# Performance work log

Measured on AMD Instinct MI355X. Metric: run time of the kernel, lower is better.

The kernel has to match this reference:

```python
import jax, jax.numpy as jnp
import numpy as np

B, M, N, R, FIN, D, H = 16, 512, 512, 8, 4, 256, 4
DH = D // H
LGAT = 2
TF_RATE, THRESH = 0.9, 2.0
GAT_W, ORG_W, DET_W = 0.5, 0.5, 0.5


def setup_inputs() -> dict:
    key = jax.random.key(0)
    ks = jax.random.split(key, 16)
    g = lambda k, shp, fan: jax.random.normal(k, shp, jnp.float32) / np.sqrt(fan)
    inp = {
        'tracks': jax.random.normal(ks[0], (B, M, R, FIN), jnp.float32),
        'detections': jax.random.normal(ks[1], (B, N, FIN), jnp.float32),
        'tracklet_marks': jax.random.randint(ks[2], (B,), M // 2, M + 1, jnp.int32),
        'detection_marks': jax.random.randint(ks[3], (B,), N // 2, N + 1, jnp.int32),
        'feat_W1': g(ks[4], (FIN, D), FIN),
        'feat_b1': jnp.zeros((D,), jnp.float32),
        'feat_W2': g(ks[5], (D, D), D),
        'feat_b2': jnp.zeros((D,), jnp.float32),
        'enc_Wqkv': g(ks[6], (D, 3 * D), D),
        'enc_Wo': g(ks[7], (D, D), D),
        'enc_ff1': g(ks[8], (D, 4 * D), D),
        'enc_ff2': g(ks[9], (4 * D, D), 4 * D),
        'gat_W': g(ks[10], (LGAT, D, D), D),
        'gat_a': g(ks[11], (LGAT, 2, H, DH), DH),
        'det_gat_W': g(ks[12], (LGAT, D, D), D),
        'det_gat_a': g(ks[13], (LGAT, 2, H, DH), DH),
        'cls_Wq': g(ks[14], (2, D, D), D),
        'cls_Wk': g(ks[15], (2, D, D), D),
    }
    return inp


def _ln(x):
    m = jnp.mean(x, -1, keepdims=True)
    v = jnp.var(x, -1, keepdims=True)
    return (x - m) * jax.lax.rsqrt(v + 1e-5)


def _feat(x, W1, b1, W2, b2):
    return jax.nn.elu(x @ W1 + b1) @ W2 + b2


def _encoder(x, Wqkv, Wo, ff1, ff2):
    # x: [T, R, D] -> one pre-LN transformer layer over the rewind axis
    T = x.shape[0]
    h = _ln(x)
    qkv = (h @ Wqkv).reshape(T, R, 3, H, DH)
    q, k, v = qkv[:, :, 0], qkv[:, :, 1], qkv[:, :, 2]
    att = jax.nn.softmax(jnp.einsum('trhd,tshd->thrs', q, k) / np.sqrt(DH), axis=-1)
    o = jnp.einsum('thrs,tshd->trhd', att, v).reshape(T, R, D) @ Wo
    x = x + o
    return x + jax.nn.relu(_ln(x) @ ff1) @ ff2


def _gat(x, adj, W, a):
    # x: [B, Nn, D]; adj: [B, Nn, Nn] bool; a: [2, H, DH]
    b, nn_, _ = x.shape
    h = (x @ W).reshape(b, nn_, H, DH)
    src = jnp.einsum('bnhd,hd->bnh', h, a[0])
    dst = jnp.einsum('bnhd,hd->bnh', h, a[1])
    e = jax.nn.leaky_relu(src[:, :, None, :] + dst[:, None, :, :], 0.2)  # [B,Nn,Nn,H]
    e = jnp.where(adj[..., None], e, -1e9)
    alpha = jax.nn.softmax(e, axis=2)
    out = jnp.einsum('bijh,bjhd->bihd', alpha, h).reshape(b, nn_, D)
    return jax.nn.elu(out)


def _scores(x, adj_f, Wq, Wk):
    s = jax.nn.sigmoid(jnp.einsum('bid,bjd->bij', x @ Wq, x @ Wk) / np.sqrt(D))
    return s * adj_f


def _forward(tracks, detections, tracklet_marks, detection_marks,
             feat_W1, feat_b1, feat_W2, feat_b2,
             enc_Wqkv, enc_Wo, enc_ff1, enc_ff2,
             gat_W, gat_a, det_gat_W, det_gat_a, cls_Wq, cls_Wk):
    tr_emb = _feat(tracks, feat_W1, feat_b1, feat_W2, feat_b2)      # [B,M,R,D]
    det_emb = _feat(detections, feat_W1, feat_b1, feat_W2, feat_b2)  # [B,N,D]

    enc = _encoder(tr_emb.reshape(B * M, R, D), enc_Wqkv, enc_Wo, enc_ff1, enc_ff2)
    enc = enc.reshape(B, M, R, D)
    predicted = tr_emb[:, :, 0, :] + TF_RATE * enc[:, :, 0, :]       # [B,M,D]

    tmask = jnp.arange(M)[None, :] < tracklet_marks[:, None]
    dmask = jnp.arange(N)[None, :] < detection_marks[:, None]

    pos = jnp.concatenate([tracks[:, :, 0, :2], detections[:, :, :2]], axis=1)  # [B,M+N,2]
    vmask = jnp.concatenate([tmask, dmask], axis=1)
    dist = jnp.linalg.norm(pos[:, :, None, :] - pos[:, None, :, :], axis=-1)
    adj = (dist < THRESH) & vmask[:, :, None] & vmask[:, None, :]
    adj_f = adj.astype(jnp.float32)

    feat0 = jnp.concatenate([predicted, det_emb], axis=1)  # [B,M+N,D]
    x = feat0
    for l in range(LGAT):
        x = GAT_W * _gat(x, adj, gat_W[l], gat_a[l]) + ORG_W * feat0
    scores = _scores(x, adj_f, cls_Wq[0], cls_Wk[0])       # [B,M+N,M+N]
    asso_results = scores[:, :M, M:]                        # track->det block

    pd = detections[:, :, :2]
    dist_d = jnp.linalg.norm(pd[:, :, None, :] - pd[:, None, :, :], axis=-1)
    adj_d = (dist_d < THRESH) & dmask[:, :, None] & dmask[:, None, :]
    adj_d_f = adj_d.astype(jnp.float32)

    xd = det_emb
    for l in range(LGAT):
        xd = DET_W * _gat(xd, adj_d, det_gat_W[l], det_gat_a[l]) + ORG_W * det_emb
    det_scores = _scores(xd, adj_d_f, cls_Wq[1], cls_Wk[1])
    det_scores = det_scores * (1.0 - jnp.eye(N, dtype=jnp.float32))  # zero_diag

    return scores, det_scores, asso_results


def reference(tracks, detections, tracklet_marks, detection_marks,
              feat_W1, feat_b1, feat_W2, feat_b2,
              enc_Wqkv, enc_Wo, enc_ff1, enc_ff2,
              gat_W, gat_a, det_gat_W, det_gat_a, cls_Wq, cls_Wk):
    return _forward(tracks, detections, tracklet_marks, detection_marks,
                    feat_W1, feat_b1, feat_W2, feat_b2,
                    enc_Wqkv, enc_Wo, enc_ff1, enc_ff2,
                    gat_W, gat_a, det_gat_W, det_gat_a, cls_Wq, cls_Wk)
```

## Files before the change

kernel.cpp:

```cpp
#include <hip/hip_runtime.h>
#include <math.h>


typedef __bf16 bf16;
typedef __bf16 bf16x8 __attribute__((ext_vector_type(8)));
typedef __bf16 bf16x4 __attribute__((ext_vector_type(4)));
typedef float f32x4 __attribute__((ext_vector_type(4)));

__device__ __forceinline__ float bf2f(bf16 x) { return (float)x; }
__device__ __forceinline__ bf16 f2bf(float x) { return (bf16)x; }

__device__ __forceinline__ unsigned encf(float f) {
    unsigned u = __float_as_uint(f);
    return (u & 0x80000000u) ? ~u : (u | 0x80000000u);
}
__device__ __forceinline__ float decf(unsigned u) {
    return (u & 0x80000000u) ? __uint_as_float(u & 0x7fffffffu)
                             : __uint_as_float(~u);
}

__device__ __forceinline__ bool node_adj(float4 a, float4 c) {
    float dx = a.x - c.x, dy = a.y - c.y;
    return (sqrtf(dx * dx + dy * dy) + a.z + c.z) < 2.0f;
}
// ... 8 lines not shown
    int k = 0;
    #pragma unroll
    for (int q = 1; q < 13; ++q) if (tid >= tab.e[q].tstart) k = q;
    PrepEnt E = tab.e[k];
    const int local = tid - E.tstart;
    const int cT = E.C >> 5;
    const int tr = local / cT, tc = local - tr * cT;
    const int r0 = tr << 5, c0 = tc << 5;
    const int t = threadIdx.x;
    {
        int r = t >> 3, cq = (t & 7) * 4;
        *(float4*)&tile[r][cq] = *(const float4*)(E.src + (long)(r0 + r) * E.C + c0 + cq);
    }
    __syncthreads();
    {
        int c = t >> 3, rq = (t & 7) * 4;
        bf16x4 o;
        o[0] = f2bf(tile[rq + 0][c]); o[1] = f2bf(tile[rq + 1][c]);
        o[2] = f2bf(tile[rq + 2][c]); o[3] = f2bf(tile[rq + 3][c]);
        *(bf16x4*)(dst + E.dofs + (long)(c0 + c) * E.R + r0 + rq) = o;
    }
}

__device__ __forceinline__ void gemm_bt(const bf16* __restrict__ A, int lda,
                                        const bf16* __restrict__ BT, int ldb,
                                        int K, f32x4 acc[4])
{
    __shared__ bf16 As[64][40];
    __shared__ bf16 Bs[64][40];
    const int t = threadIdx.x;
    const int m0 = blockIdx.y * 64;
    const int n0 = blockIdx.x * 64;
    const int lane = t & 63, wv = t >> 6, lr = lane & 15, kq = lane >> 4;
    const int arow = t >> 2, acol = (t & 3) * 8;
    for (int k0 = 0; k0 < K; k0 += 32) {
        __syncthreads();
        *(uint4*)&As[arow][acol] = *(const uint4*)(A + (long)(m0 + arow) * lda + k0 + acol);
        *(uint4*)&Bs[arow][acol] = *(const uint4*)(BT + (long)(n0 + arow) * ldb + k0 + acol);
        __syncthreads();
        bf16x8 af = *(const bf16x8*)&As[wv * 16 + lr][kq * 8];
        #pragma unroll
        for (int nt = 0; nt < 4; ++nt) {
            bf16x8 bfr = *(const bf16x8*)&Bs[nt * 16 + lr][kq * 8];
            acc[nt] = __builtin_amdgcn_mfma_f32_16x16x32_bf16(af, bfr, acc[nt], 0, 0, 0);
        }
    }
}

__device__ __forceinline__ void gemm128_core(const bf16* __restrict__ A, int lda,
                                             const bf16* __restrict__ BT, int ldb,
                                             int m0, int n0, int K, f32x4 acc[2][8])
{
    __shared__ bf16 As[128][40];
    __shared__ bf16 Bs[128][40];
    const int t = threadIdx.x;
    const int lane = t & 63, wv = t >> 6, lr = lane & 15, kq = lane >> 4;
    const int srow = t >> 1, scol = (t & 1) * 16;
    for (int k0 = 0; k0 < K; k0 += 32) {
        __syncthreads();
        {
            const bf16* ap = A + (long)(m0 + srow) * lda + k0 + scol;
            *(uint4*)&As[srow][scol] = *(const uint4*)ap;
            *(uint4*)&As[srow][scol + 8] = *(const uint4*)(ap + 8);
            const bf16* bp = BT + (long)(n0 + srow) * ldb + k0 + scol;
            *(uint4*)&Bs[srow][scol] = *(const uint4*)bp;
            *(uint4*)&Bs[srow][scol + 8] = *(const uint4*)(bp + 8);
        }
        __syncthreads();
        bf16x8 af[2];
// ... 14 lines not shown
    bf16* __restrict__ out, int ldo, int K, int relu)
{
    f32x4 acc[2][8] = {};
    const int m0 = blockIdx.y * 128, n0 = blockIdx.x * 128;
    gemm128_core(A, lda, BT, ldb, m0, n0, K, acc);
    const int lane = threadIdx.x & 63, wv = threadIdx.x >> 6;
    const int lr = lane & 15, kq = lane >> 4;
    #pragma unroll
    for (int mt = 0; mt < 2; ++mt) {
        #pragma unroll
        for (int nt = 0; nt < 8; ++nt) {
            int col = n0 + nt * 16 + lr;
            #pragma unroll
            for (int i = 0; i < 4; ++i) {
                int row = m0 + wv * 32 + mt * 16 + kq * 4 + i;
                float v = acc[mt][nt][i];
                if (relu) v = fmaxf(v, 0.f);
                out[(long)row * ldo + col] = f2bf(v);
            }
        }
    }
}

__global__ __launch_bounds__(256) void k_gemm128_logits(
    const bf16* __restrict__ xqk, long sAz, int K,
    float* __restrict__ out, int ldo, long sOz,
    const unsigned long long* __restrict__ adjm, int nN, int nC,
    float* __restrict__ asso, int flags)
{
    f32x4 acc[2][8] = {};
    const int z = blockIdx.z;
    const int m0 = blockIdx.y * 128, n0 = blockIdx.x * 128;
    gemm128_core(xqk + z * sAz, 512, xqk + z * sAz + 256, 512, m0, n0, K, acc);
    const int lane = threadIdx.x & 63, wv = threadIdx.x >> 6;
    const int lr = lane & 15, kq = lane >> 4;
    float* ob = out + z * sOz;
    #pragma unroll
    for (int mt = 0; mt < 2; ++mt) {
        #pragma unroll
        for (int i = 0; i < 4; ++i) {
            int row = m0 + wv * 32 + mt * 16 + kq * 4 + i;
            unsigned long long w0 = adjm[((long)z * nN + row) * nC + (n0 >> 6)];
            unsigned long long w1 = adjm[((long)z * nN + row) * nC + (n0 >> 6) + 1];
            #pragma unroll
            for (int nt = 0; nt < 8; ++nt) {
                int col = n0 + nt * 16 + lr;
                int bp = nt * 16 + lr;
                bool adj = (bp < 64) ? ((w0 >> bp) & 1ull) : ((w1 >> (bp - 64)) & 1ull);
                if ((flags & 2) && row == col) adj = false;
                float v = 0.f;
                if (adj) v = 1.f / (1.f + __expf(-acc[mt][nt][i] * 0.0625f));
                ob[(long)row * ldo + col] = v;
                if ((flags & 1) && row < 512 && col >= 512)
                    asso[(long)z * 262144 + (long)row * 512 + (col - 512)] = v;
            }
        }
    }
}

__global__ __launch_bounds__(256) void k_gemm_bf16(
    const bf16* __restrict__ A, int lda,
    const bf16* __restrict__ BT, int ldb,
    bf16* __restrict__ out, int ldo, int K, int relu)
{
    f32x4 acc[4] = {};
    gemm_bt(A, lda, BT, ldb, K, acc);
    const int lane = threadIdx.x & 63, wv = threadIdx.x >> 6;
    const int lr = lane & 15, kq = lane >> 4;
    const int m0 = blockIdx.y * 64, n0 = blockIdx.x * 64;
    #pragma unroll
    for (int nt = 0; nt < 4; ++nt) {
        int col = n0 + nt * 16 + lr;
        #pragma unroll
        for (int i = 0; i < 4; ++i) {
            int row = m0 + wv * 16 + kq * 4 + i;
            float v = acc[nt][i];
            if (relu) v = fmaxf(v, 0.f);
            out[(long)row * ldo + col] = f2bf(v);
        }
    }
}

__global__ __launch_bounds__(256) void k_gemm_addres(
    const bf16* __restrict__ A, int lda,
    const bf16* __restrict__ BT, int ldb,
    const float* __restrict__ res1, int ldr1,
    float* __restrict__ outf, int ldo, int K)
{
    f32x4 acc[4] = {};
    gemm_bt(A, lda, BT, ldb, K, acc);
    const int lane = threadIdx.x & 63, wv = threadIdx.x >> 6;
    const int lr = lane & 15, kq = lane >> 4;
    const int m0 = blockIdx.y * 64, n0 = blockIdx.x * 64;
    #pragma unroll
    for (int nt = 0; nt < 4; ++nt) {
        int col = n0 + nt * 16 + lr;
        #pragma unroll
        for (int i = 0; i < 4; ++i) {
            int row = m0 + wv * 16 + kq * 4 + i;
            outf[(long)row * ldo + col] = res1[(long)row * ldr1 + col] + acc[nt][i];
        }
    }
}

__global__ __launch_bounds__(256) void k_gemm_pred(
    const bf16* __restrict__ A, int lda,
    const bf16* __restrict__ BT, int ldb,
    const float* __restrict__ res1, const float* __restrict__ res2,
    float* __restrict__ outf, bf16* __restrict__ outb, int K)
{
    f32x4 acc[4] = {};
    gemm_bt(A, lda, BT, ldb, K, acc);
    const int lane = threadIdx.x & 63, wv = threadIdx.x >> 6;
    const int lr = lane & 15, kq = lane >> 4;
    const int m0 = blockIdx.y * 64, n0 = blockIdx.x * 64;
    #pragma unroll
    for (int nt = 0; nt < 4; ++nt) {
        int col = n0 + nt * 16 + lr;
        #pragma unroll
        for (int i = 0; i < 4; ++i) {
            int row = m0 + wv * 16 + kq * 4 + i;
            float v = res1[(long)row * 256 + col]
                    + 0.9f * (res2[(long)row * 256 + col] + acc[nt][i]);
            long drow = (long)row + ((row >> 9) << 9);
            long o = drow * 256 + col;
            outf[o] = v;
            outb[o] = f2bf(v);
        }
    }
}

__global__ __launch_bounds__(256) void k_gemm_T(
    const bf16* __restrict__ WT, const bf16* __restrict__ X,
    bf16* __restrict__ hgT, int nN, int nLog)
{
    f32x4 acc[4] = {};
    gemm_bt(WT, 256, X, 256, 256, acc);
    const int lane = threadIdx.x & 63, wv = threadIdx.x >> 6;
    const int lr = lane & 15, kq = lane >> 4;
    const int d0 = blockIdx.y * 64, n0 = blockIdx.x * 64;
    #pragma unroll
    for (int nt = 0; nt < 4; ++nt) {
        int node = n0 + nt * 16 + lr;
        int b = node >> nLog;
        int j = node & (nN - 1);
        #pragma unroll
        for (int i = 0; i < 4; ++i) {
            int d = d0 + wv * 16 + kq * 4 + i;
            hgT[((long)(b * 256 + d) << nLog) + j] = f2bf(acc[nt][i]);
        }
    }
}

__global__ __launch_bounds__(256) void k_featgemm(
    const float* __restrict__ tracks, const float* __restrict__ dets,
    const float* __restrict__ W1, const float* __restrict__ b1,
    const bf16* __restrict__ W2T, const float* __restrict__ b2,
    bf16* __restrict__ emb_b, float* __restrict__ emb_r0_f,
    float* __restrict__ feat0_f, bf16* __restrict__ feat0_b,
    bf16* __restrict__ demb_b)
{
    __shared__ float xr[64][4];
    __shared__ float w1s[4][256];
    __shared__ float b1s[256];
    __shared__ bf16 As[64][40];
    __shared__ bf16 Bs[256][40];
    const int t = threadIdx.x;
    const int m0 = blockIdx.x * 64;
    if (t < 64) {
        int gr = m0 + t;
        const float* sp = (gr < 65536) ? (tracks + (long)gr * 4)
                                       : (dets + (long)(gr - 65536) * 4);
        *(float4*)&xr[t][0] = *(const float4*)sp;
    }
    w1s[0][t] = W1[t];       w1s[1][t] = W1[256 + t];
    w1s[2][t] = W1[512 + t]; w1s[3][t] = W1[768 + t];
    b1s[t] = b1[t];
    const int arow = t >> 2, acol = (t & 3) * 8;
    const int lane = t & 63, wv = t >> 6, lr = lane & 15, kq = lane >> 4;
    f32x4 acc[16] = {};
    __syncthreads();
// ... 2 lines not shown
        #pragma unroll
        for (int j = 0; j < 8; ++j) {
            int c = k0 + acol + j;
            float v = fmaf(xr[arow][0], w1s[0][c],
                      fmaf(xr[arow][1], w1s[1][c],
                      fmaf(xr[arow][2], w1s[2][c],
                      fmaf(xr[arow][3], w1s[3][c], b1s[c]))));
            v = v > 0.f ? v : (__expf(v) - 1.f);
            As[arow][acol + j] = f2bf(v);
        }
        #pragma unroll
        for (int rr = 0; rr < 4; ++rr) {
            int n = rr * 64 + (t >> 2);
            *(uint4*)&Bs[n][acol] = *(const uint4*)(W2T + (long)n * 256 + k0 + acol);
        }
        __syncthreads();
        bf16x8 af = *(const bf16x8*)&As[wv * 16 + lr][kq * 8];
        #pragma unroll
        for (int nt = 0; nt < 16; ++nt) {
            bf16x8 bfr = *(const bf16x8*)&Bs[nt * 16 + lr][kq * 8];
            acc[nt] = __builtin_amdgcn_mfma_f32_16x16x32_bf16(af, bfr, acc[nt], 0, 0, 0);
        }
    }
    #pragma unroll
    for (int nt = 0; nt < 16; ++nt) {
        int col = nt * 16 + lr;
        float bv = b2[col];
        #pragma unroll
        for (int i = 0; i < 4; ++i) {
            int gr = m0 + wv * 16 + kq * 4 + i;
            float v = acc[nt][i] + bv;
            emb_b[(long)gr * 256 + col] = f2bf(v);
            if (gr < 65536) {
                if ((gr & 7) == 0) emb_r0_f[(long)(gr >> 3) * 256 + col] = v;
            } else {
                int dr = gr - 65536;
                long drow = ((long)(dr >> 9) << 10) + 512 + (dr & 511);
                feat0_f[drow * 256 + col] = v;
                feat0_b[drow * 256 + col] = f2bf(v);
                demb_b[(long)dr * 256 + col] = f2bf(v);
            }
        }
    }
}

__global__ __launch_bounds__(256) void k_adjmask(
    const float4* __restrict__ nodes,
    unsigned long long* __restrict__ adjm_main,
    unsigned long long* __restrict__ adjm_det)
{
    int bi, nN, nLog, nodeOfs;
    unsigned long long* adjm;
    if (blockIdx.x < 16384) { bi = blockIdx.x; nN = 1024; nLog = 10; nodeOfs = 0; adjm = adjm_main; }
    else { bi = blockIdx.x - 16384; nN = 512; nLog = 9; nodeOfs = 512; adjm = adjm_det; }
    const int b = bi >> nLog;
    const int i = bi & (nN - 1);
    const float4* nb = nodes + b * 1024 + nodeOfs;
    const float4 ni = nb[i];
    const int t = threadIdx.x;
    const int w = t >> 6, lane = t & 63;
    const int nC = nN >> 6;
    for (int it = 0; it * 256 < nN; ++it) {
        int j = it * 256 + t;
        bool adj = node_adj(ni, nb[j]);
        unsigned long long mask = __ballot(adj);
        if (lane == 0) adjm[(long)bi * nC + it * 4 + w] = mask;
    }
}

__global__ __launch_bounds__(256) void k_ln_bf16(const bf16* __restrict__ x, bf16* __restrict__ out)
{
    const int w = threadIdx.x >> 6, l = threadIdx.x & 63;
    const long row = (long)blockIdx.x * 4 + w;
    bf16x4 xv = *(const bf16x4*)(x + row * 256 + l * 4);
    float v0 = bf2f(xv[0]), v1 = bf2f(xv[1]), v2 = bf2f(xv[2]), v3 = bf2f(xv[3]);
    float s = v0 + v1 + v2 + v3;
    #pragma unroll
    for (int o = 32; o; o >>= 1) s += __shfl_xor(s, o, 64);
    float mean = s * (1.f / 256.f);
    float d0 = v0 - mean, d1 = v1 - mean, d2 = v2 - mean, d3 = v3 - mean;
    float q = d0 * d0 + d1 * d1 + d2 * d2 + d3 * d3;
    #pragma unroll
    for (int o = 32; o; o >>= 1) q += __shfl_xor(q, o, 64);
    float rstd = rsqrtf(q * (1.f / 256.f) + 1e-5f);
    bf16x4 ov;
    ov[0] = f2bf(d0 * rstd); ov[1] = f2bf(d1 * rstd);
    ov[2] = f2bf(d2 * rstd); ov[3] = f2bf(d3 * rstd);
    *(bf16x4*)(out + row * 256 + l * 4) = ov;
}

__global__ __launch_bounds__(256) void k_ln_f32(const float* __restrict__ x, bf16* __restrict__ out)
{
    const int w = threadIdx.x >> 6, l = threadIdx.x & 63;
    const long row = (long)blockIdx.x * 4 + w;
    float4 xv = *(const float4*)(x + row * 256 + l * 4);
    float s = xv.x + xv.y + xv.z + xv.w;
    #pragma unroll
    for (int o = 32; o; o >>= 1) s += __shfl_xor(s, o, 64);
    float mean = s * (1.f / 256.f);
    float d0 = xv.x - mean, d1 = xv.y - mean, d2 = xv.z - mean, d3 = xv.w - mean;
    float q = d0 * d0 + d1 * d1 + d2 * d2 + d3 * d3;
    #pragma unroll
    for (int o = 32; o; o >>= 1) q += __shfl_xor(q, o, 64);
    float rstd = rsqrtf(q * (1.f / 256.f) + 1e-5f);
    bf16x4 ov;
    ov[0] = f2bf(d0 * rstd); ov[1] = f2bf(d1 * rstd);
    ov[2] = f2bf(d2 * rstd); ov[3] = f2bf(d3 * rstd);
    *(bf16x4*)(out + row * 256 + l * 4) = ov;
}

__global__ __launch_bounds__(256) void k_attn(
    const bf16* __restrict__ q, const bf16* __restrict__ kv,
    bf16* __restrict__ o0)
{
    const long t = blockIdx.x;
    const int h = threadIdx.x >> 6;
    const int lane = threadIdx.x & 63;
    const int s = lane >> 3;
    const int dg = lane & 7;
    const bf16* qp = q + t * 256 + h * 64 + dg * 8;
    const bf16* kp = kv + (t * 8 + s) * 512 + h * 64 + dg * 8;
    float p = 0.f;
    #pragma unroll
    for (int e = 0; e < 8; ++e) p += bf2f(qp[e]) * bf2f(kp[e]);
    p += __shfl_xor(p, 1, 64);
    p += __shfl_xor(p, 2, 64);
    p += __shfl_xor(p, 4, 64);
    float sc = p * 0.125f;
    float w[8];
    float mx = -1e30f;
    #pragma unroll
// ... 13 lines not shown
    const float* __restrict__ tracks, const float* __restrict__ dets,
    const int* __restrict__ tm, const int* __restrict__ dm,
    float4* __restrict__ nodes, unsigned* __restrict__ maxd_all)
{
    int idx = blockIdx.x * 256 + threadIdx.x;
    if (blockIdx.x == 0) maxd_all[threadIdx.x] = 0x007fffffu;
    int b = idx >> 10;
    int i = idx & 1023;
    float x, y;
    int valid;
    if (i < 512) {
        long o = (long)(b * 512 + i) * 32;
        x = tracks[o]; y = tracks[o + 1];
        valid = (i < tm[b]) ? 1 : 0;
    } else {
        int n = i - 512;
        long o = (long)(b * 512 + n) * 4;
        x = dets[o]; y = dets[o + 1];
        valid = (n < dm[b]) ? 1 : 0;
    }
    nodes[idx] = make_float4(x, y, valid ? 0.f : 1e9f, 0.f);
}

__global__ __launch_bounds__(256) void k_srcdst_T(
    const bf16* __restrict__ hgT, const float* __restrict__ av,
    float* __restrict__ src, float* __restrict__ dst,
    unsigned* __restrict__ maxd_enc, int nN, int nLog)
{
    __shared__ float avs[512];
    const int t = threadIdx.x;
    avs[t] = av[t]; avs[256 + t] = av[256 + t];
    __syncthreads();
    const int jl = t & 63, h = t >> 6;
    const int n = blockIdx.x * 64 + jl;
    const int b = n >> nLog, j = n & (nN - 1);
    const bf16* base = hgT + (((long)b * 256 + h * 64) << nLog) + j;
    float p0 = 0.f, p1 = 0.f;
    #pragma unroll 8
    for (int dd = 0; dd < 64; ++dd) {
        float v = bf2f(base[(long)dd << nLog]);
        p0 += v * avs[h * 64 + dd];
        p1 += v * avs[256 + h * 64 + dd];
    }
    src[(long)n * 4 + h] = p0;
    dst[(long)n * 4 + h] = p1;
    float m = p1;
    #pragma unroll
    for (int o = 32; o; o >>= 1) m = fmaxf(m, __shfl_xor(m, o, 64));
    if (jl == 0) atomicMax(&maxd_enc[b * 4 + h], encf(m));
}

__global__ __launch_bounds__(256) void k_gatagg_mm(
    const bf16* __restrict__ hgT,
    const unsigned long long* __restrict__ adjm,
    const float4* __restrict__ srcv, const unsigned* __restrict__ maxd_enc,
    const float4* __restrict__ dstv,
    const float* __restrict__ res, int resBatchStride,
    bf16* __restrict__ outb, int nN)
{
    __shared__ float dstT[4][1024];
    __shared__ unsigned int adjW[32][33];
    const int t = threadIdx.x;
    const int nblk = nN >> 5;
    const int b = blockIdx.x / nblk;
    const int i0 = (blockIdx.x - b * nblk) << 5;
    const int nC = nN >> 6;
    for (int j = t; j < nN; j += 256) {
        float4 dj = dstv[(long)b * nN + j];
        dstT[0][j] = dj.x; dstT[1][j] = dj.y; dstT[2][j] = dj.z; dstT[3][j] = dj.w;
    }
    for (int idx = t; idx < 32 * nC; idx += 256) {
        int r = idx / nC, c = idx - r * nC;
        unsigned long long v = adjm[((long)b * nN + i0 + r) * nC + c];
        adjW[r][c * 2] = (unsigned)v;
        adjW[r][c * 2 + 1] = (unsigned)(v >> 32);
    }
    __syncthreads();
    const int h = t >> 6, lane = t & 63, lr = lane & 15, kq = lane >> 4;
    const float mdh = decf(maxd_enc[b * 4 + h]);
    float s_r[2], m_r[2], psum[2] = {0.f, 0.f};
    #pragma unroll
    for (int mt = 0; mt < 2; ++mt) {
        long idx = (long)b * nN + i0 + mt * 16 + lr;
        s_r[mt] = ((const float*)(srcv + idx))[h];
        float tmp = s_r[mt] + mdh;
        m_r[mt] = fmaxf(tmp, 0.2f * tmp);
    }
    f32x4 acc[2][4] = {};
    const bf16* hb = hgT + ((long)b * 256 + h * 64) * nN;
    for (int j0 = 0; j0 < nN; j0 += 32) {
        bf16x8 bfr[4];
        #pragma unroll
        for (int nt = 0; nt < 4; ++nt)
            bfr[nt] = *(const bf16x8*)(hb + (long)(nt * 16 + lr) * nN + j0 + kq * 8);
        #pragma unroll
        for (int mt = 0; mt < 2; ++mt) {
            unsigned byte = (adjW[mt * 16 + lr][j0 >> 5] >> (kq * 8)) & 0xffu;
            bf16x8 af;
            float ps = 0.f;
            #pragma unroll
            for (int jj = 0; jj < 8; ++jj) {
                float e = s_r[mt] + dstT[h][j0 + kq * 8 + jj];
// ... 10 lines not shown
        }
    }
    float stot[2];
    #pragma unroll
    for (int mt = 0; mt < 2; ++mt) {
        float v = psum[mt];
        v += __shfl_xor(v, 16, 64);
        v += __shfl_xor(v, 32, 64);
        stot[mt] = v;
    }
    #pragma unroll
    for (int mt = 0; mt < 2; ++mt) {
        #pragma unroll
        for (int ii = 0; ii < 4; ++ii) {
            int i = i0 + mt * 16 + kq * 4 + ii;
            long bi = (long)b * nN + i;
            float sv = __shfl(stot[mt], kq * 4 + ii, 64);
            float rs = 1.f / fmaxf(sv, 1e-30f);
            #pragma unroll
            for (int nt = 0; nt < 4; ++nt) {
                int col = h * 64 + nt * 16 + lr;
                float a = acc[mt][nt][ii] * rs;
                float e = a > 0.f ? a : expm1f(a);
                float v = 0.5f * e + 0.5f * res[(long)b * resBatchStride + (long)i * 256 + col];
                outb[bi * 256 + col] = f2bf(v);
            }
        }
    }
}

extern "C" void kernel_launch(void* const* d_in, const int* in_sizes, int n_in,
                              void* d_out, int out_size, void* d_ws, size_t ws_size,
                              hipStream_t stream)
{
    (void)in_sizes; (void)n_in; (void)out_size; (void)ws_size;
    const float* tracks = (const float*)d_in[0];
    const float* dets   = (const float*)d_in[1];
    const int*  tmarks = (const int*)d_in[2];
    const int*  dmarks = (const int*)d_in[3];
    const float* W1   = (const float*)d_in[4];
    const float* b1   = (const float*)d_in[5];
    const float* W2   = (const float*)d_in[6];
    const float* b2   = (const float*)d_in[7];
    const float* Wqkv = (const float*)d_in[8];
    const float* Wo   = (const float*)d_in[9];
    const float* eff1 = (const float*)d_in[10];
    const float* eff2 = (const float*)d_in[11];
// ... 9 lines not shown
    size_t off = 0;
    auto take = [&](size_t bytes) -> char* {
        char* p = wsb + off;
        off += (bytes + 255) & ~(size_t)255;
        return p;
    };
    char* R_emb  = take(37748736);
    char* R_r0   = take(8388608);
    char* R_hln  = take(33554432);
    char* R_v    = take(33554432);
    char* R_gat  = take(25165824);
    char* R_q    = take(4194304);
    char* R_o0   = take(4194304);
    char* R_f0f  = take(16777216);
    char* R_f0b  = take(8388608);
    char* R_demb = take(4194304);
    float4* nodes = (float4*)take(262144);
    float4* src4  = (float4*)take(262144);
    float4* dst4  = (float4*)take(262144);
    unsigned* maxd_all = (unsigned*)take(1024);
    unsigned long long* adjm_main = (unsigned long long*)take(2097152);
    unsigned long long* adjm_det  = (unsigned long long*)take(524288);
    bf16* wbuf = (bf16*)take(2752512);

    bf16*  emb_b    = (bf16*)R_emb;
    float* emb_r0_f = (float*)R_r0;
    bf16*  hln      = (bf16*)R_hln;
    bf16*  kv_b     = (bf16*)d_out;
    bf16*  q_b      = (bf16*)R_q;
    bf16*  o0_b     = (bf16*)R_o0;
    float* x20      = (float*)R_emb;
    bf16*  h2_b     = (bf16*)(R_emb + 8388608);
    bf16*  f1_b     = (bf16*)R_hln;
    float* feat0_f  = (float*)R_f0f;
    bf16*  feat0_b  = (bf16*)R_f0b;
    bf16*  demb_b   = (bf16*)R_demb;
    bf16*  hgT      = (bf16*)R_gat;
    bf16*  xga_b    = (bf16*)(R_gat + 8388608);
    bf16*  xgb_b    = (bf16*)(R_gat + 16777216);
    bf16*  xqk_b    = (bf16*)R_v;

    bf16* W2T    = wbuf + 0;
    bf16* WqkvT  = wbuf + 65536;
    bf16* WoT    = wbuf + 262144;
    bf16* eff1T  = wbuf + 327680;
    bf16* eff2T  = wbuf + 589824;
    bf16* gatW0T = wbuf + 851968;
    bf16* gatW1T = wbuf + 917504;
    bf16* dgatW0T= wbuf + 983040;
    bf16* dgatW1T= wbuf + 1048576;
    bf16* clsQK0T= wbuf + 1114112;
    bf16* clsQK1T= wbuf + 1245184;
    PrepTab tab;
    tab.e[0]  = { W2,             0,       256,  256,  0    };
    tab.e[1]  = { Wqkv,           65536,   256,  768,  64   };
    tab.e[2]  = { Wo,             262144,  256,  256,  256  };
    tab.e[3]  = { eff1,           327680,  256,  1024, 320  };
    tab.e[4]  = { eff2,           589824,  1024, 256,  576  };
    tab.e[5]  = { gatW,           851968,  256,  256,  832  };
    tab.e[6]  = { gatW + 65536,   917504,  256,  256,  896  };
    tab.e[7]  = { dgatW,          983040,  256,  256,  960  };
    tab.e[8]  = { dgatW + 65536,  1048576, 256,  256,  1024 };
    tab.e[9]  = { clsWq,          1114112, 256,  256,  1088 };
    tab.e[10] = { clsWk,          1179648, 256,  256,  1152 };
    tab.e[11] = { clsWq + 65536,  1245184, 256,  256,  1216 };
    tab.e[12] = { clsWk + 65536,  1310720, 256,  256,  1280 };

    k_prep<<<1344, 256, 0, stream>>>(tab, wbuf);
    k_nodes<<<64, 256, 0, stream>>>(tracks, dets, tmarks, dmarks, nodes, maxd_all);
    k_adjmask<<<24576, 256, 0, stream>>>(nodes, adjm_main, adjm_det);
    k_featgemm<<<1152, 256, 0, stream>>>(tracks, dets, W1, b1, W2T, b2,
        emb_b, emb_r0_f, feat0_f, feat0_b, demb_b);

    k_ln_bf16<<<16384, 256, 0, stream>>>(emb_b, hln);
    k_gemm128_bf16<<<dim3(4, 512, 1), 256, 0, stream>>>(hln, 256, WqkvT + 65536, 256, kv_b, 512, 256, 0);
    k_gemm_bf16<<<dim3(4, 128, 1), 256, 0, stream>>>(hln, 2048, WqkvT, 256, q_b, 256, 256, 0);
    k_attn<<<8192, 256, 0, stream>>>(q_b, kv_b, o0_b);
    k_gemm_addres<<<dim3(4, 128, 1), 256, 0, stream>>>(o0_b, 256, WoT, 256, emb_r0_f, 256, x20, 256, 256);
    k_ln_f32<<<2048, 256, 0, stream>>>(x20, h2_b);
    k_gemm128_bf16<<<dim3(8, 64, 1), 256, 0, stream>>>(h2_b, 256, eff1T, 256, f1_b, 1024, 256, 1);
    k_gemm_pred<<<dim3(4, 128, 1), 256, 0, stream>>>(f1_b, 1024, eff2T, 1024, emb_r0_f, x20, feat0_f, feat0_b, 1024);

    k_gemm_T<<<dim3(256, 4, 1), 256, 0, stream>>>(gatW0T, feat0_b, hgT, 1024, 10);
    k_srcdst_T<<<256, 256, 0, stream>>>(hgT, gatA, (float*)src4, (float*)dst4, maxd_all, 1024, 10);
    k_gatagg_mm<<<512, 256, 0, stream>>>(hgT, adjm_main, src4, maxd_all, dst4,
        feat0_f, 262144, xga_b, 1024);
    k_gemm_T<<<dim3(256, 4, 1), 256, 0, stream>>>(gatW1T, xga_b, hgT, 1024, 10);
    k_srcdst_T<<<256, 256, 0, stream>>>(hgT, gatA + 512, (float*)src4, (float*)dst4, maxd_all + 64, 1024, 10);
    k_gatagg_mm<<<512, 256, 0, stream>>>(hgT, adjm_main, src4, maxd_all + 64, dst4,
        feat0_f, 262144, xgb_b, 1024);
    k_gemm_bf16<<<dim3(8, 256, 1), 256, 0, stream>>>(xgb_b, 256, clsQK0T, 256, xqk_b, 512, 256, 0);
    k_gemm128_logits<<<dim3(8, 8, 16), 256, 0, stream>>>(xqk_b, 524288L, 256,
        out, 1024, 1048576L, adjm_main, 1024, 16, out + 20971520L, 1);

    k_gemm_T<<<dim3(128, 4, 1), 256, 0, stream>>>(dgatW0T, demb_b, hgT, 512, 9);
    k_srcdst_T<<<128, 256, 0, stream>>>(hgT, dgatA, (float*)src4, (float*)dst4, maxd_all + 128, 512, 9);
    k_gatagg_mm<<<256, 256, 0, stream>>>(hgT, adjm_det, src4, maxd_all + 128, dst4,
        feat0_f + 131072, 262144, xga_b, 512);
    k_gemm_T<<<dim3(128, 4, 1), 256, 0, stream>>>(dgatW1T, xga_b, hgT, 512, 9);
    k_srcdst_T<<<128, 256, 0, stream>>>(hgT, dgatA + 512, (float*)src4, (float*)dst4, maxd_all + 192, 512, 9);
    k_gatagg_mm<<<256, 256, 0, stream>>>(hgT, adjm_det, src4, maxd_all + 192, dst4,
        feat0_f + 131072, 262144, xgb_b, 512);
    k_gemm_bf16<<<dim3(8, 128, 1), 256, 0, stream>>>(xgb_b, 256, clsQK1T, 256, xqk_b, 512, 256, 0);
    k_gemm128_logits<<<dim3(4, 4, 16), 256, 0, stream>>>(xqk_b, 262144L, 256,
        out + 16777216L, 512, 262144L, adjm_det, 512, 8, (float*)nullptr, 2);
}
```

Measured before the change: 588.6 us.

## Fuse LayerNorms into GEMM epilogues and batch track/detection GAT branches

```diff
diff --git a/kernel.cpp b/kernel.cpp
--- a/kernel.cpp
+++ b/kernel.cpp
@@ -54,15 +54,13 @@
     }
 }
 
-__device__ __forceinline__ void gemm_bt(const bf16* __restrict__ A, int lda,
-                                        const bf16* __restrict__ BT, int ldb,
-                                        int K, f32x4 acc[4])
+__device__ __forceinline__ void gemm_bt_mn(const bf16* __restrict__ A, int lda,
+                                           const bf16* __restrict__ BT, int ldb,
+                                           int K, int m0, int n0, f32x4 acc[4])
 {
     __shared__ bf16 As[64][40];
     __shared__ bf16 Bs[64][40];
     const int t = threadIdx.x;
-    const int m0 = blockIdx.y * 64;
-    const int n0 = blockIdx.x * 64;
     const int lane = t & 63, wv = t >> 6, lr = lane & 15, kq = lane >> 4;
     const int arow = t >> 2, acol = (t & 3) * 8;
     for (int k0 = 0; k0 < K; k0 += 32) {
@@ -77,6 +75,13 @@
             acc[nt] = __builtin_amdgcn_mfma_f32_16x16x32_bf16(af, bfr, acc[nt], 0, 0, 0);
         }
     }
+}
+
+__device__ __forceinline__ void gemm_bt(const bf16* __restrict__ A, int lda,
+                                        const bf16* __restrict__ BT, int ldb,
+                                        int K, f32x4 acc[4])
+{
+    gemm_bt_mn(A, lda, BT, ldb, K, blockIdx.y * 64, blockIdx.x * 64, acc);
 }
 
 __device__ __forceinline__ void gemm128_core(const bf16* __restrict__ A, int lda,
@@ -137,19 +142,68 @@
     }
 }
 
-__global__ __launch_bounds__(256) void k_gemm128_logits(
-    const bf16* __restrict__ xqk, long sAz, int K,
-    float* __restrict__ out, int ldo, long sOz,
-    const unsigned long long* __restrict__ adjm, int nN, int nC,
-    float* __restrict__ asso, int flags)
-{
+__global__ __launch_bounds__(256) void k_kvq(
+    const bf16* __restrict__ hln, const bf16* __restrict__ WqkvT,
+    bf16* __restrict__ kv, bf16* __restrict__ q)
+{
+    const int bid = blockIdx.x;
+    const bf16* A; const bf16* BT; bf16* out;
+    int lda, ldo, m0, n0;
+    if (bid < 2048) {
+        A = hln; lda = 256; BT = WqkvT + 65536;
+        m0 = (bid >> 2) * 128; n0 = (bid & 3) * 128;
+        out = kv; ldo = 512;
+    } else {
+        int t2 = bid - 2048;
+        A = hln; lda = 2048; BT = WqkvT;
+        m0 = (t2 >> 1) * 128; n0 = (t2 & 1) * 128;
+        out = q; ldo = 256;
+    }
     f32x4 acc[2][8] = {};
-    const int z = blockIdx.z;
-    const int m0 = blockIdx.y * 128, n0 = blockIdx.x * 128;
-    gemm128_core(xqk + z * sAz, 512, xqk + z * sAz + 256, 512, m0, n0, K, acc);
+    gemm128_core(A, lda, BT, 256, m0, n0, 256, acc);
     const int lane = threadIdx.x & 63, wv = threadIdx.x >> 6;
     const int lr = lane & 15, kq = lane >> 4;
-    float* ob = out + z * sOz;
+    #pragma unroll
+    for (int mt = 0; mt < 2; ++mt) {
+        #pragma unroll
+        for (int nt = 0; nt < 8; ++nt) {
+            int col = n0 + nt * 16 + lr;
+            #pragma unroll
+            for (int i = 0; i < 4; ++i) {
+                int row = m0 + wv * 32 + mt * 16 + kq * 4 + i;
+                out[(long)row * ldo + col] = f2bf(acc[mt][nt][i]);
+            }
+        }
+    }
+}
+
+__global__ __launch_bounds__(256) void k_logits(
+    const bf16* __restrict__ xqkm, const bf16* __restrict__ xqkd,
+    const unsigned long long* __restrict__ adjmM,
+    const unsigned long long* __restrict__ adjmD,
+    float* __restrict__ out, float* __restrict__ asso)
+{
+    const int bid = blockIdx.x;
+    const bf16* xqk; float* ob; const unsigned long long* adjm;
+    int ldo, nN, nC, flags, m0, n0, z;
+    long sAz, sOz;
+    if (bid < 1024) {
+        z = bid >> 6; int r = bid & 63;
+        m0 = (r >> 3) * 128; n0 = (r & 7) * 128;
+        xqk = xqkm; sAz = 524288; ob = out; ldo = 1024; sOz = 1048576;
+        adjm = adjmM; nN = 1024; nC = 16; flags = 1;
+    } else {
+        int b2 = bid - 1024;
+        z = b2 >> 4; int r = b2 & 15;
+        m0 = (r >> 2) * 128; n0 = (r & 3) * 128;
+        xqk = xqkd; sAz = 262144; ob = out + 16777216; ldo = 512; sOz = 262144;
+        adjm = adjmD; nN = 512; nC = 8; flags = 2;
+    }
+    f32x4 acc[2][8] = {};
+    gemm128_core(xqk + z * sAz, 512, xqk + z * sAz + 256, 512, m0, n0, 256, acc);
+    const int lane = threadIdx.x & 63, wv = threadIdx.x >> 6;
+    const int lr = lane & 15, kq = lane >> 4;
+    float* obz = ob + z * sOz;
     #pragma unroll
     for (int mt = 0; mt < 2; ++mt) {
         #pragma unroll
@@ -165,7 +219,7 @@
                 if ((flags & 2) && row == col) adj = false;
                 float v = 0.f;
                 if (adj) v = 1.f / (1.f + __expf(-acc[mt][nt][i] * 0.0625f));
-                ob[(long)row * ldo + col] = v;
+                obz[(long)row * ldo + col] = v;
                 if ((flags & 1) && row < 512 && col >= 512)
                     asso[(long)z * 262144 + (long)row * 512 + (col - 512)] = v;
             }
@@ -173,47 +227,26 @@
     }
 }
 
-__global__ __launch_bounds__(256) void k_gemm_bf16(
-    const bf16* __restrict__ A, int lda,
-    const bf16* __restrict__ BT, int ldb,
-    bf16* __restrict__ out, int ldo, int K, int relu)
-{
+__global__ __launch_bounds__(256) void k_cls(
+    const bf16* __restrict__ Am, const bf16* __restrict__ QKm, bf16* __restrict__ outm,
+    const bf16* __restrict__ Ad, const bf16* __restrict__ QKd, bf16* __restrict__ outd)
+{
+    int by = blockIdx.y;
+    const bf16 *A, *BT; bf16* out;
+    if (by < 256) { A = Am; BT = QKm; out = outm; }
+    else          { by -= 256; A = Ad; BT = QKd; out = outd; }
     f32x4 acc[4] = {};
-    gemm_bt(A, lda, BT, ldb, K, acc);
+    const int m0 = by * 64, n0 = blockIdx.x * 64;
+    gemm_bt_mn(A, 256, BT, 256, 256, m0, n0, acc);
     const int lane = threadIdx.x & 63, wv = threadIdx.x >> 6;
     const int lr = lane & 15, kq = lane >> 4;
-    const int m0 = blockIdx.y * 64, n0 = blockIdx.x * 64;
     #pragma unroll
     for (int nt = 0; nt < 4; ++nt) {
         int col = n0 + nt * 16 + lr;
         #pragma unroll
         for (int i = 0; i < 4; ++i) {
             int row = m0 + wv * 16 + kq * 4 + i;
-            float v = acc[nt][i];
-            if (relu) v = fmaxf(v, 0.f);
-            out[(long)row * ldo + col] = f2bf(v);
-        }
-    }
-}
-
-__global__ __launch_bounds__(256) void k_gemm_addres(
-    const bf16* __restrict__ A, int lda,
-    const bf16* __restrict__ BT, int ldb,
-    const float* __restrict__ res1, int ldr1,
-    float* __restrict__ outf, int ldo, int K)
-{
-    f32x4 acc[4] = {};
-    gemm_bt(A, lda, BT, ldb, K, acc);
-    const int lane = threadIdx.x & 63, wv = threadIdx.x >> 6;
-    const int lr = lane & 15, kq = lane >> 4;
-    const int m0 = blockIdx.y * 64, n0 = blockIdx.x * 64;
-    #pragma unroll
-    for (int nt = 0; nt < 4; ++nt) {
-        int col = n0 + nt * 16 + lr;
-        #pragma unroll
-        for (int i = 0; i < 4; ++i) {
-            int row = m0 + wv * 16 + kq * 4 + i;
-            outf[(long)row * ldo + col] = res1[(long)row * ldr1 + col] + acc[nt][i];
+            out[(long)row * 512 + col] = f2bf(acc[nt][i]);
         }
     }
 }
@@ -245,33 +278,11 @@
     }
 }
 
-__global__ __launch_bounds__(256) void k_gemm_T(
-    const bf16* __restrict__ WT, const bf16* __restrict__ X,
-    bf16* __restrict__ hgT, int nN, int nLog)
-{
-    f32x4 acc[4] = {};
-    gemm_bt(WT, 256, X, 256, 256, acc);
-    const int lane = threadIdx.x & 63, wv = threadIdx.x >> 6;
-    const int lr = lane & 15, kq = lane >> 4;
-    const int d0 = blockIdx.y * 64, n0 = blockIdx.x * 64;
-    #pragma unroll
-    for (int nt = 0; nt < 4; ++nt) {
-        int node = n0 + nt * 16 + lr;
-        int b = node >> nLog;
-        int j = node & (nN - 1);
-        #pragma unroll
-        for (int i = 0; i < 4; ++i) {
-            int d = d0 + wv * 16 + kq * 4 + i;
-            hgT[((long)(b * 256 + d) << nLog) + j] = f2bf(acc[nt][i]);
-        }
-    }
-}
-
 __global__ __launch_bounds__(256) void k_featgemm(
     const float* __restrict__ tracks, const float* __restrict__ dets,
     const float* __restrict__ W1, const float* __restrict__ b1,
     const bf16* __restrict__ W2T, const float* __restrict__ b2,
-    bf16* __restrict__ emb_b, float* __restrict__ emb_r0_f,
+    bf16* __restrict__ hln, float* __restrict__ emb_r0_f,
     float* __restrict__ feat0_f, bf16* __restrict__ feat0_b,
     bf16* __restrict__ demb_b)
 {
@@ -320,18 +331,55 @@
             acc[nt] = __builtin_amdgcn_mfma_f32_16x16x32_bf16(af, bfr, acc[nt], 0, 0, 0);
         }
     }
-    #pragma unroll
-    for (int nt = 0; nt < 16; ++nt) {
-        int col = nt * 16 + lr;
-        float bv = b2[col];
+    if (m0 < 65536) {
+        #pragma unroll
+        for (int nt = 0; nt < 16; ++nt) {
+            int col = nt * 16 + lr;
+            float bv = b2[col];
+            #pragma unroll
+            for (int i = 0; i < 4; ++i) {
+                int gr = m0 + wv * 16 + kq * 4 + i;
+                float v = acc[nt][i] + bv;
+                if ((gr & 7) == 0) emb_r0_f[(long)(gr >> 3) * 256 + col] = v;
+                acc[nt][i] = bf2f(f2bf(v));
+            }
+        }
+        float mean[4], rstd[4];
         #pragma unroll
         for (int i = 0; i < 4; ++i) {
-            int gr = m0 + wv * 16 + kq * 4 + i;
-            float v = acc[nt][i] + bv;
-            emb_b[(long)gr * 256 + col] = f2bf(v);
-            if (gr < 65536) {
-                if ((gr & 7) == 0) emb_r0_f[(long)(gr >> 3) * 256 + col] = v;
-            } else {
+            float s1 = 0.f, s2 = 0.f;
+            #pragma unroll
+            for (int nt = 0; nt < 16; ++nt) {
+                float v = acc[nt][i];
+                s1 += v; s2 += v * v;
+            }
+            #pragma unroll
+            for (int o = 1; o < 16; o <<= 1) {
+                s1 += __shfl_xor(s1, o, 64);
+                s2 += __shfl_xor(s2, o, 64);
+            }
+            float mu = s1 * (1.f / 256.f);
+            mean[i] = mu;
+            rstd[i] = rsqrtf(fmaxf(s2 * (1.f / 256.f) - mu * mu, 0.f) + 1e-5f);
+        }
+        #pragma unroll
+        for (int nt = 0; nt < 16; ++nt) {
+            int col = nt * 16 + lr;
+            #pragma unroll
+            for (int i = 0; i < 4; ++i) {
+                int gr = m0 + wv * 16 + kq * 4 + i;
+                hln[(long)gr * 256 + col] = f2bf((acc[nt][i] - mean[i]) * rstd[i]);
+            }
+        }
+    } else {
+        #pragma unroll
+        for (int nt = 0; nt < 16; ++nt) {
+            int col = nt * 16 + lr;
+            float bv = b2[col];
+            #pragma unroll
+            for (int i = 0; i < 4; ++i) {
+                int gr = m0 + wv * 16 + kq * 4 + i;
+                float v = acc[nt][i] + bv;
                 int dr = gr - 65536;
                 long drow = ((long)(dr >> 9) << 10) + 512 + (dr & 511);
                 feat0_f[drow * 256 + col] = v;
@@ -366,45 +414,65 @@
     }
 }
 
-__global__ __launch_bounds__(256) void k_ln_bf16(const bf16* __restrict__ x, bf16* __restrict__ out)
-{
-    const int w = threadIdx.x >> 6, l = threadIdx.x & 63;
-    const long row = (long)blockIdx.x * 4 + w;
-    bf16x4 xv = *(const bf16x4*)(x + row * 256 + l * 4);
-    float v0 = bf2f(xv[0]), v1 = bf2f(xv[1]), v2 = bf2f(xv[2]), v3 = bf2f(xv[3]);
-    float s = v0 + v1 + v2 + v3;
-    #pragma unroll
-    for (int o = 32; o; o >>= 1) s += __shfl_xor(s, o, 64);
-    float mean = s * (1.f / 256.f);
-    float d0 = v0 - mean, d1 = v1 - mean, d2 = v2 - mean, d3 = v3 - mean;
-    float q = d0 * d0 + d1 * d1 + d2 * d2 + d3 * d3;
-    #pragma unroll
-    for (int o = 32; o; o >>= 1) q += __shfl_xor(q, o, 64);
-    float rstd = rsqrtf(q * (1.f / 256.f) + 1e-5f);
-    bf16x4 ov;
-    ov[0] = f2bf(d0 * rstd); ov[1] = f2bf(d1 * rstd);
-    ov[2] = f2bf(d2 * rstd); ov[3] = f2bf(d3 * rstd);
-    *(bf16x4*)(out + row * 256 + l * 4) = ov;
-}
-
-__global__ __launch_bounds__(256) void k_ln_f32(const float* __restrict__ x, bf16* __restrict__ out)
-{
-    const int w = threadIdx.x >> 6, l = threadIdx.x & 63;
-    const long row = (long)blockIdx.x * 4 + w;
-    float4 xv = *(const float4*)(x + row * 256 + l * 4);
-    float s = xv.x + xv.y + xv.z + xv.w;
-    #pragma unroll
-    for (int o = 32; o; o >>= 1) s += __shfl_xor(s, o, 64);
-    float mean = s * (1.f / 256.f);
-    float d0 = xv.x - mean, d1 = xv.y - mean, d2 = xv.z - mean, d3 = xv.w - mean;
-    float q = d0 * d0 + d1 * d1 + d2 * d2 + d3 * d3;
-    #pragma unroll
-    for (int o = 32; o; o >>= 1) q += __shfl_xor(q, o, 64);
-    float rstd = rsqrtf(q * (1.f / 256.f) + 1e-5f);
-    bf16x4 ov;
-    ov[0] = f2bf(d0 * rstd); ov[1] = f2bf(d1 * rstd);
-    ov[2] = f2bf(d2 * rstd); ov[3] = f2bf(d3 * rstd);
-    *(bf16x4*)(out + row * 256 + l * 4) = ov;
+__global__ __launch_bounds__(256) void k_addres_ln(
+    const bf16* __restrict__ A, const bf16* __restrict__ BT,
+    const float* __restrict__ res1,
+    float* __restrict__ x2out, bf16* __restrict__ h2)
+{
+    __shared__ bf16 As[64][40];
+    __shared__ bf16 Bs[256][40];
+    const int t = threadIdx.x;
+    const int m0 = blockIdx.x * 64;
+    const int arow = t >> 2, acol = (t & 3) * 8;
+    const int lane = t & 63, wv = t >> 6, lr = lane & 15, kq = lane >> 4;
+    f32x4 acc[16] = {};
+    for (int k0 = 0; k0 < 256; k0 += 32) {
+        __syncthreads();
+        *(uint4*)&As[arow][acol] = *(const uint4*)(A + (long)(m0 + arow) * 256 + k0 + acol);
+        #pragma unroll
+        for (int rr = 0; rr < 4; ++rr) {
+            int n = rr * 64 + (t >> 2);
+            *(uint4*)&Bs[n][acol] = *(const uint4*)(BT + (long)n * 256 + k0 + acol);
+        }
+        __syncthreads();
+        bf16x8 af = *(const bf16x8*)&As[wv * 16 + lr][kq * 8];
+        #pragma unroll
+        for (int nt = 0; nt < 16; ++nt) {
+            bf16x8 bfr = *(const bf16x8*)&Bs[nt * 16 + lr][kq * 8];
+            acc[nt] = __builtin_amdgcn_mfma_f32_16x16x32_bf16(af, bfr, acc[nt], 0, 0, 0);
+        }
+    }
+    float mean[4], rstd[4];
+    #pragma unroll
+    for (int i = 0; i < 4; ++i) {
+        int row = m0 + wv * 16 + kq * 4 + i;
+        float s1 = 0.f, s2 = 0.f;
+        #pragma unroll
+        for (int nt = 0; nt < 16; ++nt) {
+            float v = res1[(long)row * 256 + nt * 16 + lr] + acc[nt][i];
+            acc[nt][i] = v;
+            s1 += v; s2 += v * v;
+        }
+        #pragma unroll
+        for (int o = 1; o < 16; o <<= 1) {
+            s1 += __shfl_xor(s1, o, 64);
+            s2 += __shfl_xor(s2, o, 64);
+        }
+        float mu = s1 * (1.f / 256.f);
+        mean[i] = mu;
+        rstd[i] = rsqrtf(fmaxf(s2 * (1.f / 256.f) - mu * mu, 0.f) + 1e-5f);
+    }
+    #pragma unroll
+    for (int nt = 0; nt < 16; ++nt) {
+        int col = nt * 16 + lr;
+        #pragma unroll
+        for (int i = 0; i < 4; ++i) {
+            int row = m0 + wv * 16 + kq * 4 + i;
+            float v = acc[nt][i];
+            x2out[(long)row * 256 + col] = v;
+            h2[(long)row * 256 + col] = f2bf((v - mean[i]) * rstd[i]);
+        }
+    }
 }
 
 __global__ __launch_bounds__(256) void k_attn(
@@ -464,48 +532,80 @@
     nodes[idx] = make_float4(x, y, valid ? 0.f : 1e9f, 0.f);
 }
 
-__global__ __launch_bounds__(256) void k_srcdst_T(
-    const bf16* __restrict__ hgT, const float* __restrict__ av,
-    float* __restrict__ src, float* __restrict__ dst,
-    unsigned* __restrict__ maxd_enc, int nN, int nLog)
-{
-    __shared__ float avs[512];
-    const int t = threadIdx.x;
-    avs[t] = av[t]; avs[256 + t] = av[256 + t];
+__global__ __launch_bounds__(256) void k_gemmT_src(
+    const bf16* __restrict__ WTm, const bf16* __restrict__ Xm, bf16* __restrict__ hgTm,
+    const float* __restrict__ avm, float* __restrict__ srcm, float* __restrict__ dstm,
+    unsigned* __restrict__ mxm,
+    const bf16* __restrict__ WTd, const bf16* __restrict__ Xd, bf16* __restrict__ hgTd,
+    const float* __restrict__ avd, float* __restrict__ srcd, float* __restrict__ dstd,
+    unsigned* __restrict__ mxd)
+{
+    __shared__ float sred[4][2][64];
+    int bx = blockIdx.x;
+    const bf16 *WT, *X; bf16* hgT; const float* av;
+    float *src, *dst; unsigned* mx; int nN, nLog;
+    if (bx < 256) { WT = WTm; X = Xm; hgT = hgTm; av = avm; src = srcm; dst = dstm; mx = mxm; nN = 1024; nLog = 10; }
+    else { bx -= 256; WT = WTd; X = Xd; hgT = hgTd; av = avd; src = srcd; dst = dstd; mx = mxd; nN = 512; nLog = 9; }
+    const int h = blockIdx.y;
+    const int d0 = h * 64, n0 = bx * 64;
+    f32x4 acc[4] = {};
+    gemm_bt_mn(WT, 256, X, 256, 256, d0, n0, acc);
+    const int t = threadIdx.x, lane = t & 63, wv = t >> 6, lr = lane & 15, kq = lane >> 4;
+    float a0c[4], a1c[4];
+    *(float4*)a0c = *(const float4*)(av + h * 64 + wv * 16 + kq * 4);
+    *(float4*)a1c = *(const float4*)(av + 256 + h * 64 + wv * 16 + kq * 4);
+    #pragma unroll
+    for (int nt = 0; nt < 4; ++nt) {
+        int node = n0 + nt * 16 + lr;
+        int b = node >> nLog;
+        int j = node & (nN - 1);
+        float p0 = 0.f, p1 = 0.f;
+        #pragma unroll
+        for (int i = 0; i < 4; ++i) {
+            int d = d0 + wv * 16 + kq * 4 + i;
+            bf16 vb = f2bf(acc[nt][i]);
+            hgT[((long)(b * 256 + d) << nLog) + j] = vb;
+            float vr = bf2f(vb);
+            p0 += vr * a0c[i];
+            p1 += vr * a1c[i];
+        }
+        p0 += __shfl_xor(p0, 16, 64); p0 += __shfl_xor(p0, 32, 64);
+        p1 += __shfl_xor(p1, 16, 64); p1 += __shfl_xor(p1, 32, 64);
+        if (kq == 0) { sred[wv][0][nt * 16 + lr] = p0; sred[wv][1][nt * 16 + lr] = p1; }
+    }
     __syncthreads();
-    const int jl = t & 63, h = t >> 6;
-    const int n = blockIdx.x * 64 + jl;
-    const int b = n >> nLog, j = n & (nN - 1);
-    const bf16* base = hgT + (((long)b * 256 + h * 64) << nLog) + j;
-    float p0 = 0.f, p1 = 0.f;
-    #pragma unroll 8
-    for (int dd = 0; dd < 64; ++dd) {
-        float v = bf2f(base[(long)dd << nLog]);
-        p0 += v * avs[h * 64 + dd];
-        p1 += v * avs[256 + h * 64 + dd];
-    }
-    src[(long)n * 4 + h] = p0;
-    dst[(long)n * 4 + h] = p1;
-    float m = p1;
-    #pragma unroll
-    for (int o = 32; o; o >>= 1) m = fmaxf(m, __shfl_xor(m, o, 64));
-    if (jl == 0) atomicMax(&maxd_enc[b * 4 + h], encf(m));
-}
-
-__global__ __launch_bounds__(256) void k_gatagg_mm(
-    const bf16* __restrict__ hgT,
-    const unsigned long long* __restrict__ adjm,
-    const float4* __restrict__ srcv, const unsigned* __restrict__ maxd_enc,
-    const float4* __restrict__ dstv,
-    const float* __restrict__ res, int resBatchStride,
-    bf16* __restrict__ outb, int nN)
+    if (t < 64) {
+        float s0 = sred[0][0][t] + sred[1][0][t] + sred[2][0][t] + sred[3][0][t];
+        float s1 = sred[0][1][t] + sred[1][1][t] + sred[2][1][t] + sred[3][1][t];
+        int node = n0 + t;
+        src[(long)node * 4 + h] = s0;
+        dst[(long)node * 4 + h] = s1;
+        float m = s1;
+        #pragma unroll
+        for (int o = 32; o; o >>= 1) m = fmaxf(m, __shfl_xor(m, o, 64));
+        if (t == 0) atomicMax(&mx[(n0 >> nLog) * 4 + h], encf(m));
+    }
+}
+
+__global__ __launch_bounds__(256) void k_gatagg2(
+    const bf16* __restrict__ hgTm, const unsigned long long* __restrict__ adjmM,
+    const float4* __restrict__ srcM, const unsigned* __restrict__ mxM,
+    const float4* __restrict__ dstM, const float* __restrict__ resM, bf16* __restrict__ outM,
+    const bf16* __restrict__ hgTd, const unsigned long long* __restrict__ adjmD,
+    const float4* __restrict__ srcD, const unsigned* __restrict__ mxD,
+    const float4* __restrict__ dstD, const float* __restrict__ resD, bf16* __restrict__ outD)
 {
     __shared__ float dstT[4][1024];
     __shared__ unsigned int adjW[32][33];
+    int bid = blockIdx.x;
+    const bf16* hgT; const unsigned long long* adjm; const float4* srcv;
+    const unsigned* mxp; const float4* dstv; const float* res; bf16* outb; int nN;
+    if (bid < 512) { hgT = hgTm; adjm = adjmM; srcv = srcM; mxp = mxM; dstv = dstM; res = resM; outb = outM; nN = 1024; }
+    else { bid -= 512; hgT = hgTd; adjm = adjmD; srcv = srcD; mxp = mxD; dstv = dstD; res = resD; outb = outD; nN = 512; }
     const int t = threadIdx.x;
     const int nblk = nN >> 5;
-    const int b = blockIdx.x / nblk;
-    const int i0 = (blockIdx.x - b * nblk) << 5;
+    const int b = bid / nblk;
+    const int i0 = (bid - b * nblk) << 5;
     const int nC = nN >> 6;
     for (int j = t; j < nN; j += 256) {
         float4 dj = dstv[(long)b * nN + j];
@@ -519,7 +619,7 @@
     }
     __syncthreads();
     const int h = t >> 6, lane = t & 63, lr = lane & 15, kq = lane >> 4;
-    const float mdh = decf(maxd_enc[b * 4 + h]);
+    const float mdh = decf(mxp[b * 4 + h]);
     float s_r[2], m_r[2], psum[2] = {0.f, 0.f};
     #pragma unroll
     for (int mt = 0; mt < 2; ++mt) {
@@ -576,7 +676,7 @@
                 int col = h * 64 + nt * 16 + lr;
                 float a = acc[mt][nt][ii] * rs;
                 float e = a > 0.f ? a : expm1f(a);
-                float v = 0.5f * e + 0.5f * res[(long)b * resBatchStride + (long)i * 256 + col];
+                float v = 0.5f * e + 0.5f * res[(long)b * 262144 + (long)i * 256 + col];
                 outb[bi * 256 + col] = f2bf(v);
             }
         }
@@ -632,8 +732,9 @@
     unsigned long long* adjm_main = (unsigned long long*)take(2097152);
     unsigned long long* adjm_det  = (unsigned long long*)take(524288);
     bf16* wbuf = (bf16*)take(2752512);
-
-    bf16*  emb_b    = (bf16*)R_emb;
+    float4* srcd4 = (float4*)take(131072);
+    float4* dstd4 = (float4*)take(131072);
+
     float* emb_r0_f = (float*)R_r0;
     bf16*  hln      = (bf16*)R_hln;
     bf16*  kv_b     = (bf16*)d_out;
@@ -645,10 +746,14 @@
     float* feat0_f  = (float*)R_f0f;
     bf16*  feat0_b  = (bf16*)R_f0b;
     bf16*  demb_b   = (bf16*)R_demb;
-    bf16*  hgT      = (bf16*)R_gat;
-    bf16*  xga_b    = (bf16*)(R_gat + 8388608);
-    bf16*  xgb_b    = (bf16*)(R_gat + 16777216);
-    bf16*  xqk_b    = (bf16*)R_v;
+    bf16*  hgT_m    = (bf16*)R_gat;
+    bf16*  xga_m    = (bf16*)(R_gat + 8388608);
+    bf16*  xgb_m    = (bf16*)(R_gat + 16777216);
+    bf16*  hgT_d    = (bf16*)(R_emb + 16777216);
+    bf16*  xga_d    = (bf16*)(R_emb + 20971520);
+    bf16*  xgb_d    = (bf16*)(R_emb + 25165824);
+    bf16*  xqk_m    = (bf16*)R_v;
+    bf16*  xqk_d    = (bf16*)(R_v + 16777216);
 
     bf16* W2T    = wbuf + 0;
     bf16* WqkvT  = wbuf + 65536;
@@ -680,38 +785,28 @@
     k_nodes<<<64, 256, 0, stream>>>(tracks, dets, tmarks, dmarks, nodes, maxd_all);
     k_adjmask<<<24576, 256, 0, stream>>>(nodes, adjm_main, adjm_det);
     k_featgemm<<<1152, 256, 0, stream>>>(tracks, dets, W1, b1, W2T, b2,
-        emb_b, emb_r0_f, feat0_f, feat0_b, demb_b);
-
-    k_ln_bf16<<<16384, 256, 0, stream>>>(emb_b, hln);
-    k_gemm128_bf16<<<dim3(4, 512, 1), 256, 0, stream>>>(hln, 256, WqkvT + 65536, 256, kv_b, 512, 256, 0);
-    k_gemm_bf16<<<dim3(4, 128, 1), 256, 0, stream>>>(hln, 2048, WqkvT, 256, q_b, 256, 256, 0);
+        hln, emb_r0_f, feat0_f, feat0_b, demb_b);
+
+    k_kvq<<<2176, 256, 0, stream>>>(hln, WqkvT, kv_b, q_b);
     k_attn<<<8192, 256, 0, stream>>>(q_b, kv_b, o0_b);
-    k_gemm_addres<<<dim3(4, 128, 1), 256, 0, stream>>>(o0_b, 256, WoT, 256, emb_r0_f, 256, x20, 256, 256);
-    k_ln_f32<<<2048, 256, 0, stream>>>(x20, h2_b);
+    k_addres_ln<<<128, 256, 0, stream>>>(o0_b, WoT, emb_r0_f, x20, h2_b);
     k_gemm128_bf16<<<dim3(8, 64, 1), 256, 0, stream>>>(h2_b, 256, eff1T, 256, f1_b, 1024, 256, 1);
     k_gemm_pred<<<dim3(4, 128, 1), 256, 0, stream>>>(f1_b, 1024, eff2T, 1024, emb_r0_f, x20, feat0_f, feat0_b, 1024);
 
-    k_gemm_T<<<dim3(256, 4, 1), 256, 0, stream>>>(gatW0T, feat0_b, hgT, 1024, 10);
-    k_srcdst_T<<<256, 256, 0, stream>>>(hgT, gatA, (float*)src4, (float*)dst4, maxd_all, 1024, 10);
-    k_gatagg_mm<<<512, 256, 0, stream>>>(hgT, adjm_main, src4, maxd_all, dst4,
-        feat0_f, 262144, xga_b, 1024);
-    k_gemm_T<<<dim3(256, 4, 1), 256, 0, stream>>>(gatW1T, xga_b, hgT, 1024, 10);
-    k_srcdst_T<<<256, 256, 0, stream>>>(hgT, gatA + 512, (float*)src4, (float*)dst4, maxd_all + 64, 1024, 10);
-    k_gatagg_mm<<<512, 256, 0, stream>>>(hgT, adjm_main, src4, maxd_all + 64, dst4,
-        feat0_f, 262144, xgb_b, 1024);
-    k_gemm_bf16<<<dim3(8, 256, 1), 256, 0, stream>>>(xgb_b, 256, clsQK0T, 256, xqk_b, 512, 256, 0);
-    k_gemm128_logits<<<dim3(8, 8, 16), 256, 0, stream>>>(xqk_b, 524288L, 256,
-        out, 1024, 1048576L, adjm_main, 1024, 16, out + 20971520L, 1);
-
-    k_gemm_T<<<dim3(128, 4, 1), 256, 0, stream>>>(dgatW0T, demb_b, hgT, 512, 9);
-    k_srcdst_T<<<128, 256, 0, stream>>>(hgT, dgatA, (float*)src4, (float*)dst4, maxd_all + 128, 512, 9);
-    k_gatagg_mm<<<256, 256, 0, stream>>>(hgT, adjm_det, src4, maxd_all + 128, dst4,
-        feat0_f + 131072, 262144, xga_b, 512);
-    k_gemm_T<<<dim3(128, 4, 1), 256, 0, stream>>>(dgatW1T, xga_b, hgT, 512, 9);
-    k_srcdst_T<<<128, 256, 0, stream>>>(hgT, dgatA + 512, (float*)src4, (float*)dst4, maxd_all + 192, 512, 9);
-    k_gatagg_mm<<<256, 256, 0, stream>>>(hgT, adjm_det, src4, maxd_all + 192, dst4,
-        feat0_f + 131072, 262144, xgb_b, 512);
-    k_gemm_bf16<<<dim3(8, 128, 1), 256, 0, stream>>>(xgb_b, 256, clsQK1T, 256, xqk_b, 512, 256, 0);
-    k_gemm128_logits<<<dim3(4, 4, 16), 256, 0, stream>>>(xqk_b, 262144L, 256,
-        out + 16777216L, 512, 262144L, adjm_det, 512, 8, (float*)nullptr, 2);
-}
+    k_gemmT_src<<<dim3(384, 4, 1), 256, 0, stream>>>(
+        gatW0T, feat0_b, hgT_m, gatA, (float*)src4, (float*)dst4, maxd_all,
+        dgatW0T, demb_b, hgT_d, dgatA, (float*)srcd4, (float*)dstd4, maxd_all + 128);
+    k_gatagg2<<<768, 256, 0, stream>>>(
+        hgT_m, adjm_main, src4, maxd_all, dst4, feat0_f, xga_m,
+        hgT_d, adjm_det, srcd4, maxd_all + 128, dstd4, feat0_f + 131072, xga_d);
+    k_gemmT_src<<<dim3(384, 4, 1), 256, 0, stream>>>(
+        gatW1T, xga_m, hgT_m, gatA + 512, (float*)src4, (float*)dst4, maxd_all + 64,
+        dgatW1T, xga_d, hgT_d, dgatA + 512, (float*)srcd4, (float*)dstd4, maxd_all + 192);
+    k_gatagg2<<<768, 256, 0, stream>>>(
+        hgT_m, adjm_main, src4, maxd_all + 64, dst4, feat0_f, xgb_m,
+        hgT_d, adjm_det, srcd4, maxd_all + 192, dstd4, feat0_f + 131072, xgb_d);
+
+    k_cls<<<dim3(8, 384, 1), 256, 0, stream>>>(xgb_m, clsQK0T, xqk_m, xgb_d, clsQK1T, xqk_d);
+    k_logits<<<1280, 256, 0, stream>>>(xqk_m, xqk_d, adjm_main, adjm_det,
+        out, out + 20971520L);
+}
```

New measurement: 498.8 us. 1.18x faster.
